# Kernel optimization log

Hardware: AMD Instinct MI355X
Metric: run time of the kernel (lower is better)

The kernel has to match this reference:

```python
import jax, jax.numpy as jnp
import numpy as np

SAMPLE_RATE = 4096.0  # matches init_kwargs sample_rate
STATE_DIM = 64
LENGTH, CHANNELS = 8192, 512


def setup_inputs() -> dict:
    key = jax.random.key(0)
    kx, kc = jax.random.split(key)
    x = jax.random.normal(kx, (LENGTH, CHANNELS), dtype=jnp.float32)
    # param init exactly as in the flax module
    logA = jnp.log(1.0 + jnp.arange(STATE_DIM, dtype=jnp.float32))
    B = jnp.ones((STATE_DIM,), dtype=jnp.float32)
    C = 0.01 * jax.random.normal(kc, (STATE_DIM,), dtype=jnp.float32)  # nn.initializers.normal() stddev=0.01
    return {"x": x, "logA": logA, "B": B, "C": C}


def reference(x, logA, B, C):
    # ZOH-style discretization: A = -exp(logA); Abar = exp(A*dt); Bbar = (Abar-1)*B/A
    dt = 1.0 / SAMPLE_RATE
    A = -jnp.exp(logA)                # (N,)
    Abar = jnp.exp(A * dt)            # (N,)
    Bbar = (Abar - 1.0) * B / A       # (N,)

    channels = x.shape[1]
    h0 = jnp.zeros((channels, logA.shape[0]), dtype=x.dtype)  # (C, N)

    def step(h, xt):
        # h: (C, N), xt: (C,)
        h = Abar[None, :] * h + xt[:, None] * Bbar[None, :]
        y = h @ C                      # (C,)
        return h, y

    _, y = jax.lax.scan(step, h0, x)   # y: (L, C)
    return y
```

## Files before the change

### kernel.cpp

```cpp
#include <hip/hip_runtime.h>
#include <math.h>

#define LENGTH   8192
#define CHANNELS 512
#define NSTATE   64
#define TCHUNK   64
#define NCHUNK   (LENGTH / TCHUNK)
#define LOG2E    1.4426950408889634f
#define DT       (1.0f / 4096.0f)


__device__ __forceinline__ float lane_bcast_f(float v, int lane) {
    return __int_as_float(__builtin_amdgcn_readlane(__float_as_int(v), lane));
}

__global__ __launch_bounds__(256, 2) void k_pass1(const float* __restrict__ x,
                                                  const float* __restrict__ logA,
                                                  float* __restrict__ E) {
    int tid  = threadIdx.x;
    int k    = blockIdx.x >> 2;
    int c    = ((blockIdx.x & 3) << 7) + (tid & 127);
    int half = tid >> 7;
    int lane = tid & 63;

    int   nme = (half << 5) + (lane & 31);
    float Av  = -expf(logA[nme]);
    float abv = exp2f(Av * DT * LOG2E);

    float a[32];
    #pragma unroll
    for (int i = 0; i < 32; ++i) a[i] = lane_bcast_f(abv, i);

    float h[32];
    #pragma unroll
    for (int i = 0; i < 32; ++i) h[i] = 0.f;

    const float* xp = x + (size_t)k * TCHUNK * CHANNELS + c;
    float xv = xp[0];
    #pragma unroll 7
    for (int t = 0; t < TCHUNK - 1; ++t) {
        float xn = xp[(size_t)(t + 1) * CHANNELS];
        #pragma unroll
        for (int i = 0; i < 32; ++i) h[i] = fmaf(a[i], h[i], xv);
        xv = xn;
    }
    #pragma unroll
    for (int i = 0; i < 32; ++i) h[i] = fmaf(a[i], h[i], xv);

    float* Ep = E + ((size_t)k * NSTATE + (half << 5)) * CHANNELS + c;
    #pragma unroll
    for (int i = 0; i < 32; ++i) Ep[(size_t)i * CHANNELS] = h[i];
}

#define G2 16
__global__ __launch_bounds__(64, 1) void k_pass2(float* __restrict__ W,
                                                 const float* __restrict__ logA) {
    int gtid = blockIdx.x * 64 + threadIdx.x;
    int c = gtid & (CHANNELS - 1);
    int n = gtid >> 9;
    float A  = -expf(logA[n]);
    float aT = exp2f(A * (64.0f * DT) * LOG2E);
    float* p = W + (size_t)n * CHANNELS + c;
    const size_t S = (size_t)NSTATE * CHANNELS;

    float e[2][G2];
    #pragma unroll
    for (int j = 0; j < G2; ++j) e[0][j] = p[(size_t)j * S];

    float hc = 0.f;
    #pragma unroll
    for (int k0 = 0; k0 < NCHUNK; k0 += G2) {
        const int cur = (k0 / G2) & 1;
        const int nxt = cur ^ 1;
        if (k0 + G2 < NCHUNK) {
            #pragma unroll
            for (int j = 0; j < G2; ++j) e[nxt][j] = p[(size_t)(k0 + G2 + j) * S];
        }
        #pragma unroll
        for (int j = 0; j < G2; ++j) {
            p[(size_t)(k0 + j) * S] = hc;
            hc = fmaf(aT, hc, e[cur][j]);
        }
    }
}

__global__ __launch_bounds__(256, 2) void k_pass3(const float* __restrict__ x,
                                                  const float* __restrict__ logA,
                                                  const float* __restrict__ Bv,
                                                  const float* __restrict__ Cv,
                                                  const float* __restrict__ W,
                                                  float* __restrict__ y) {
    __shared__ float yp[2][TCHUNK][128];
    int tid  = threadIdx.x;
    int k    = blockIdx.x >> 2;
    int c0g  = (blockIdx.x & 3) << 7;
    int cl   = tid & 127;
    int c    = c0g + cl;
    int half = tid >> 7;
    int lane = tid & 63;

    int   nme  = (half << 5) + (lane & 31);
    float Av   = -expf(logA[nme]);
    float abv  = exp2f(Av * DT * LOG2E);
    float Bbar = expm1f(Av * DT) * Bv[nme] / Av;
    float cbv  = Cv[nme] * Bbar;

    float a[32], cb[32];
    #pragma unroll
    for (int i = 0; i < 32; ++i) {
        a[i]  = lane_bcast_f(abv, i);
        cb[i] = lane_bcast_f(cbv, i);
    }

    const float* Wp = W + ((size_t)k * NSTATE + (half << 5)) * CHANNELS + c;
    float h[32];
    #pragma unroll
    for (int i = 0; i < 32; ++i) h[i] = Wp[(size_t)i * CHANNELS];

    const float* xp = x + (size_t)k * TCHUNK * CHANNELS + c;
    float* ypb = &yp[half][0][cl];

    float xv = xp[0];
    #pragma unroll 3
    for (int t = 0; t < TCHUNK - 1; ++t) {
        float xn = xp[(size_t)(t + 1) * CHANNELS];
        float y0 = 0.f, y1 = 0.f, y2 = 0.f, y3 = 0.f;
        #pragma unroll
        for (int i = 0; i < 32; i += 4) {
            h[i]   = fmaf(a[i],   h[i],   xv);  y0 = fmaf(cb[i],   h[i],   y0);
            h[i+1] = fmaf(a[i+1], h[i+1], xv);  y1 = fmaf(cb[i+1], h[i+1], y1);
            h[i+2] = fmaf(a[i+2], h[i+2], xv);  y2 = fmaf(cb[i+2], h[i+2], y2);
            h[i+3] = fmaf(a[i+3], h[i+3], xv);  y3 = fmaf(cb[i+3], h[i+3], y3);
        }
        ypb[t * 128] = (y0 + y1) + (y2 + y3);
        xv = xn;
    }
    {
        float y0 = 0.f, y1 = 0.f, y2 = 0.f, y3 = 0.f;
        #pragma unroll
        for (int i = 0; i < 32; i += 4) {
            h[i]   = fmaf(a[i],   h[i],   xv);  y0 = fmaf(cb[i],   h[i],   y0);
            h[i+1] = fmaf(a[i+1], h[i+1], xv);  y1 = fmaf(cb[i+1], h[i+1], y1);
            h[i+2] = fmaf(a[i+2], h[i+2], xv);  y2 = fmaf(cb[i+2], h[i+2], y2);
            h[i+3] = fmaf(a[i+3], h[i+3], xv);  y3 = fmaf(cb[i+3], h[i+3], y3);
        }
        ypb[(TCHUNK - 1) * 128] = (y0 + y1) + (y2 + y3);
    }
    __syncthreads();

    float* yg = y + (size_t)k * TCHUNK * CHANNELS + c0g;
    #pragma unroll
    for (int i = 0; i < 8; ++i) {
        int idx = (i << 8) + tid;
        int t   = idx >> 5;
        int cq  = (idx & 31) << 2;
        float4 v0 = *(const float4*)&yp[0][t][cq];
        float4 v1 = *(const float4*)&yp[1][t][cq];
        *(float4*)(yg + (size_t)t * CHANNELS + cq) =
            make_float4(v0.x + v1.x, v0.y + v1.y, v0.z + v1.z, v0.w + v1.w);
    }
}

extern "C" void kernel_launch(void* const* d_in, const int* in_sizes, int n_in,
                              void* d_out, int out_size, void* d_ws, size_t ws_size,
                              hipStream_t stream) {
    const float* x    = (const float*)d_in[0];
    const float* logA = (const float*)d_in[1];
    const float* B    = (const float*)d_in[2];
    const float* C    = (const float*)d_in[3];
    float* yout = (float*)d_out;

    float* W = yout;
    (void)d_ws; (void)ws_size;

    k_pass1<<<NCHUNK * 4, 256, 0, stream>>>(x, logA, W);
    k_pass2<<<(NSTATE * CHANNELS) / 64, 64, 0, stream>>>(W, logA);
    k_pass3<<<NCHUNK * 4, 256, 0, stream>>>(x, logA, B, C, W, yout);
}
```

Before: 103.2 us.

## Retile chunked SSM scan: larger time chunks, 4-way state split, LDS-staged x

Doubles the time chunk to 128, which halves the number of chunk carries that pass 2 must scan and store. Passes 1 and 3 now split the 64 states across four wavefronts of 16 states over 64-channel tiles, and stage each x tile in shared memory with float4 loads. Pass 3 writes y in 32-step sub-tiles reduced across the four state groups. The carry buffer moves from the output to the workspace, with a slow per-channel fallback kernel when the workspace is too small. This adds more cross-wave reduction traffic and more syncs, and the fallback would be very slow if it ever runs.

```diff
diff --git a/kernel.cpp b/kernel.cpp
--- a/kernel.cpp
+++ b/kernel.cpp
@@ -4,8 +4,12 @@
 #define LENGTH   8192
 #define CHANNELS 512
 #define NSTATE   64
-#define TCHUNK   64
+#define TCHUNK   128
 #define NCHUNK   (LENGTH / TCHUNK)
+#define CTILE    64
+#define NQ       4
+#define TTILE    32
+#define E_ELEMS  (NCHUNK * NSTATE * CHANNELS)
 #define LOG2E    1.4426950408889634f
 #define DT       (1.0f / 4096.0f)
 
@@ -14,52 +18,59 @@
     return __int_as_float(__builtin_amdgcn_readlane(__float_as_int(v), lane));
 }
 
-__global__ __launch_bounds__(256, 2) void k_pass1(const float* __restrict__ x,
+__global__ __launch_bounds__(256, 4) void k_pass1(const float* __restrict__ x,
                                                   const float* __restrict__ logA,
                                                   float* __restrict__ E) {
-    int tid  = threadIdx.x;
-    int k    = blockIdx.x >> 2;
-    int c    = ((blockIdx.x & 3) << 7) + (tid & 127);
-    int half = tid >> 7;
-    int lane = tid & 63;
-
-    int   nme = (half << 5) + (lane & 31);
+    __shared__ float Xl[TCHUNK * CTILE];
+    int tid = threadIdx.x;
+    int k   = blockIdx.x >> 3;
+    int ct  = blockIdx.x & 7;
+    int cl  = tid & 63;
+    int q   = tid >> 6;
+    int c0g = ct * CTILE;
+
+    const float* xsrc = x + (size_t)k * TCHUNK * CHANNELS + c0g;
+    #pragma unroll
+    for (int i = 0; i < 8; ++i) {
+        int idx = (i << 8) + tid;
+        int t   = idx >> 4;
+        int cq  = (idx & 15) << 2;
+        *(float4*)&Xl[t * CTILE + cq] = *(const float4*)(xsrc + (size_t)t * CHANNELS + cq);
+    }
+
+    int   nme = (q << 4) + (cl & 15);
     float Av  = -expf(logA[nme]);
     float abv = exp2f(Av * DT * LOG2E);
-
-    float a[32];
-    #pragma unroll
-    for (int i = 0; i < 32; ++i) a[i] = lane_bcast_f(abv, i);
-
-    float h[32];
-    #pragma unroll
-    for (int i = 0; i < 32; ++i) h[i] = 0.f;
-
-    const float* xp = x + (size_t)k * TCHUNK * CHANNELS + c;
-    float xv = xp[0];
-    #pragma unroll 7
-    for (int t = 0; t < TCHUNK - 1; ++t) {
-        float xn = xp[(size_t)(t + 1) * CHANNELS];
+    float a[16];
+    #pragma unroll
+    for (int i = 0; i < 16; ++i) a[i] = lane_bcast_f(abv, i);
+
+    float h[16];
+    #pragma unroll
+    for (int i = 0; i < 16; ++i) h[i] = 0.f;
+
+    __syncthreads();
+
+    #pragma unroll 8
+    for (int t = 0; t < TCHUNK; ++t) {
+        float xv = Xl[t * CTILE + cl];
         #pragma unroll
-        for (int i = 0; i < 32; ++i) h[i] = fmaf(a[i], h[i], xv);
-        xv = xn;
-    }
-    #pragma unroll
-    for (int i = 0; i < 32; ++i) h[i] = fmaf(a[i], h[i], xv);
-
-    float* Ep = E + ((size_t)k * NSTATE + (half << 5)) * CHANNELS + c;
-    #pragma unroll
-    for (int i = 0; i < 32; ++i) Ep[(size_t)i * CHANNELS] = h[i];
+        for (int i = 0; i < 16; ++i) h[i] = fmaf(a[i], h[i], xv);
+    }
+
+    float* Ep = E + ((size_t)k * NSTATE + (q << 4)) * CHANNELS + c0g + cl;
+    #pragma unroll
+    for (int i = 0; i < 16; ++i) Ep[(size_t)i * CHANNELS] = h[i];
 }
 
 #define G2 16
-__global__ __launch_bounds__(64, 1) void k_pass2(float* __restrict__ W,
-                                                 const float* __restrict__ logA) {
-    int gtid = blockIdx.x * 64 + threadIdx.x;
+__global__ __launch_bounds__(256, 1) void k_pass2(float* __restrict__ W,
+                                                  const float* __restrict__ logA) {
+    int gtid = blockIdx.x * 256 + threadIdx.x;
     int c = gtid & (CHANNELS - 1);
     int n = gtid >> 9;
     float A  = -expf(logA[n]);
-    float aT = exp2f(A * (64.0f * DT) * LOG2E);
+    float aT = exp2f(A * ((float)TCHUNK * DT) * LOG2E);
     float* p = W + (size_t)n * CHANNELS + c;
     const size_t S = (size_t)NSTATE * CHANNELS;
 
@@ -90,74 +101,104 @@
                                                   const float* __restrict__ Cv,
                                                   const float* __restrict__ W,
                                                   float* __restrict__ y) {
-    __shared__ float yp[2][TCHUNK][128];
-    int tid  = threadIdx.x;
-    int k    = blockIdx.x >> 2;
-    int c0g  = (blockIdx.x & 3) << 7;
-    int cl   = tid & 127;
-    int c    = c0g + cl;
-    int half = tid >> 7;
-    int lane = tid & 63;
-
-    int   nme  = (half << 5) + (lane & 31);
+    __shared__ float Xl[TCHUNK * CTILE];
+    __shared__ float yp[NQ][TTILE][CTILE];
+    int tid = threadIdx.x;
+    int k   = blockIdx.x >> 3;
+    int ct  = blockIdx.x & 7;
+    int cl  = tid & 63;
+    int q   = tid >> 6;
+    int c0g = ct * CTILE;
+
+    const float* xsrc = x + (size_t)k * TCHUNK * CHANNELS + c0g;
+    #pragma unroll
+    for (int i = 0; i < 8; ++i) {
+        int idx = (i << 8) + tid;
+        int t   = idx >> 4;
+        int cq  = (idx & 15) << 2;
+        *(float4*)&Xl[t * CTILE + cq] = *(const float4*)(xsrc + (size_t)t * CHANNELS + cq);
+    }
+
+    int   nme  = (q << 4) + (cl & 15);
     float Av   = -expf(logA[nme]);
     float abv  = exp2f(Av * DT * LOG2E);
     float Bbar = expm1f(Av * DT) * Bv[nme] / Av;
     float cbv  = Cv[nme] * Bbar;
 
-    float a[32], cb[32];
-    #pragma unroll
-    for (int i = 0; i < 32; ++i) {
+    float a[16], cb[16];
+    #pragma unroll
+    for (int i = 0; i < 16; ++i) {
         a[i]  = lane_bcast_f(abv, i);
         cb[i] = lane_bcast_f(cbv, i);
     }
 
-    const float* Wp = W + ((size_t)k * NSTATE + (half << 5)) * CHANNELS + c;
-    float h[32];
-    #pragma unroll
-    for (int i = 0; i < 32; ++i) h[i] = Wp[(size_t)i * CHANNELS];
-
-    const float* xp = x + (size_t)k * TCHUNK * CHANNELS + c;
-    float* ypb = &yp[half][0][cl];
-
-    float xv = xp[0];
-    #pragma unroll 3
-    for (int t = 0; t < TCHUNK - 1; ++t) {
-        float xn = xp[(size_t)(t + 1) * CHANNELS];
-        float y0 = 0.f, y1 = 0.f, y2 = 0.f, y3 = 0.f;
+    const float* Wp = W + ((size_t)k * NSTATE + (q << 4)) * CHANNELS + c0g + cl;
+    float h[16];
+    #pragma unroll
+    for (int i = 0; i < 16; ++i) h[i] = Wp[(size_t)i * CHANNELS];
+
+    __syncthreads();
+
+    float* yg = y + (size_t)k * TCHUNK * CHANNELS + c0g;
+    #pragma unroll
+    for (int tt = 0; tt < TCHUNK / TTILE; ++tt) {
+        #pragma unroll 4
+        for (int t = 0; t < TTILE; ++t) {
+            float xv = Xl[(tt * TTILE + t) * CTILE + cl];
+            float y0 = 0.f, y1 = 0.f, y2 = 0.f, y3 = 0.f;
+            #pragma unroll
+            for (int i = 0; i < 16; i += 4) {
+                h[i]   = fmaf(a[i],   h[i],   xv);  y0 = fmaf(cb[i],   h[i],   y0);
+                h[i+1] = fmaf(a[i+1], h[i+1], xv);  y1 = fmaf(cb[i+1], h[i+1], y1);
+                h[i+2] = fmaf(a[i+2], h[i+2], xv);  y2 = fmaf(cb[i+2], h[i+2], y2);
+                h[i+3] = fmaf(a[i+3], h[i+3], xv);  y3 = fmaf(cb[i+3], h[i+3], y3);
+            }
+            yp[q][t][cl] = (y0 + y1) + (y2 + y3);
+        }
+        __syncthreads();
         #pragma unroll
-        for (int i = 0; i < 32; i += 4) {
-            h[i]   = fmaf(a[i],   h[i],   xv);  y0 = fmaf(cb[i],   h[i],   y0);
-            h[i+1] = fmaf(a[i+1], h[i+1], xv);  y1 = fmaf(cb[i+1], h[i+1], y1);
-            h[i+2] = fmaf(a[i+2], h[i+2], xv);  y2 = fmaf(cb[i+2], h[i+2], y2);
-            h[i+3] = fmaf(a[i+3], h[i+3], xv);  y3 = fmaf(cb[i+3], h[i+3], y3);
-        }
-        ypb[t * 128] = (y0 + y1) + (y2 + y3);
-        xv = xn;
-    }
-    {
-        float y0 = 0.f, y1 = 0.f, y2 = 0.f, y3 = 0.f;
-        #pragma unroll
-        for (int i = 0; i < 32; i += 4) {
-            h[i]   = fmaf(a[i],   h[i],   xv);  y0 = fmaf(cb[i],   h[i],   y0);
-            h[i+1] = fmaf(a[i+1], h[i+1], xv);  y1 = fmaf(cb[i+1], h[i+1], y1);
-            h[i+2] = fmaf(a[i+2], h[i+2], xv);  y2 = fmaf(cb[i+2], h[i+2], y2);
-            h[i+3] = fmaf(a[i+3], h[i+3], xv);  y3 = fmaf(cb[i+3], h[i+3], y3);
-        }
-        ypb[(TCHUNK - 1) * 128] = (y0 + y1) + (y2 + y3);
-    }
-    __syncthreads();
-
-    float* yg = y + (size_t)k * TCHUNK * CHANNELS + c0g;
-    #pragma unroll
-    for (int i = 0; i < 8; ++i) {
-        int idx = (i << 8) + tid;
-        int t   = idx >> 5;
-        int cq  = (idx & 31) << 2;
-        float4 v0 = *(const float4*)&yp[0][t][cq];
-        float4 v1 = *(const float4*)&yp[1][t][cq];
-        *(float4*)(yg + (size_t)t * CHANNELS + cq) =
-            make_float4(v0.x + v1.x, v0.y + v1.y, v0.z + v1.z, v0.w + v1.w);
+        for (int r = 0; r < 2; ++r) {
+            int idx = (r << 8) + tid;
+            int t   = idx >> 4;
+            int cq  = (idx & 15) << 2;
+            float4 v0 = *(const float4*)&yp[0][t][cq];
+            float4 v1 = *(const float4*)&yp[1][t][cq];
+            float4 v2 = *(const float4*)&yp[2][t][cq];
+            float4 v3 = *(const float4*)&yp[3][t][cq];
+            *(float4*)(yg + (size_t)(tt * TTILE + t) * CHANNELS + cq) =
+                make_float4((v0.x + v1.x) + (v2.x + v3.x),
+                            (v0.y + v1.y) + (v2.y + v3.y),
+                            (v0.z + v1.z) + (v2.z + v3.z),
+                            (v0.w + v1.w) + (v2.w + v3.w));
+        }
+        __syncthreads();
+    }
+}
+
+__global__ __launch_bounds__(256) void k_fallback(const float* __restrict__ x,
+                                                  const float* __restrict__ logA,
+                                                  const float* __restrict__ B,
+                                                  const float* __restrict__ C,
+                                                  float* __restrict__ y) {
+    int c = blockIdx.x * blockDim.x + threadIdx.x;
+    if (c >= CHANNELS) return;
+    float Abar[NSTATE], CB[NSTATE], h[NSTATE];
+    for (int n = 0; n < NSTATE; ++n) {
+        float A    = -expf(logA[n]);
+        float ab   = exp2f(A * DT * LOG2E);
+        float Bbar = expm1f(A * DT) * B[n] / A;
+        Abar[n] = ab;
+        CB[n]   = C[n] * Bbar;
+        h[n]    = 0.f;
+    }
+    for (int t = 0; t < LENGTH; ++t) {
+        float xv = x[(size_t)t * CHANNELS + c];
+        float acc = 0.f;
+        for (int n = 0; n < NSTATE; ++n) {
+            h[n] = fmaf(Abar[n], h[n], xv);
+            acc  = fmaf(CB[n], h[n], acc);
+        }
+        y[(size_t)t * CHANNELS + c] = acc;
     }
 }
 
@@ -170,10 +211,13 @@
     const float* C    = (const float*)d_in[3];
     float* yout = (float*)d_out;
 
-    float* W = yout;
-    (void)d_ws; (void)ws_size;
-
-    k_pass1<<<NCHUNK * 4, 256, 0, stream>>>(x, logA, W);
-    k_pass2<<<(NSTATE * CHANNELS) / 64, 64, 0, stream>>>(W, logA);
-    k_pass3<<<NCHUNK * 4, 256, 0, stream>>>(x, logA, B, C, W, yout);
-}
+    if (ws_size < (size_t)E_ELEMS * sizeof(float)) {
+        k_fallback<<<(CHANNELS + 255) / 256, 256, 0, stream>>>(x, logA, B, C, yout);
+        return;
+    }
+    float* W = (float*)d_ws;
+
+    k_pass1<<<NCHUNK * 8, 256, 0, stream>>>(x, logA, W);
+    k_pass2<<<(NSTATE * CHANNELS) / 256, 256, 0, stream>>>(W, logA);
+    k_pass3<<<NCHUNK * 8, 256, 0, stream>>>(x, logA, B, C, W, yout);
+}
```

Result: faster. 99.29 us (-3.8%).
